# Performance work log

Measured on AMD Instinct MI355X. Metric: run time of the kernel, lower is better.

The kernel has to match this reference:

```python
import jax, jax.numpy as jnp
import numpy as np

# Emphasis(alpha=0.85): y[n] = x[n] - alpha*x[n-1], implemented (as in the original
# module) via a generic STFT-domain time-varying LFilter with n_fft=512, hop=256,
# normalization (torch.istft-style). Since n_fft == win_length, the per-frame
# convolution is circular within each frame, matching the original's framing.
N_FFT = 512
HOP = 256
WIN = 512
ALPHA = 0.85


def setup_inputs() -> dict:
    key = jax.random.key(0)
    x = jax.random.normal(key, (8, 1, 2097152), dtype=jnp.float32)
    coeffs = jnp.array([1.0, -ALPHA], dtype=jnp.float32)  # registered buffer [1, -alpha]
    return {"x": x, "coeffs": coeffs}


def _lfilter_fir(x, coeffs):
    # x: (B, C, T); coeffs: (2,) FIR numerator, constant across frames
    B, C, T = x.shape
    n_frames = -(-T // HOP)  # ceil_division(T, hop)
    pad_left = WIN // 2      # centered framing
    needed = (n_frames - 1) * HOP + WIN
    pad_right = max(needed - (pad_left + T), 0) + HOP
    xp = jnp.pad(x, ((0, 0), (0, 0), (pad_left, pad_right)))
    Lp = xp.shape[-1]

    n = jnp.arange(WIN, dtype=jnp.float32)
    window = 0.5 - 0.5 * jnp.cos(2.0 * jnp.pi * n / WIN)  # periodic Hann (torch.hann_window)

    idx = jnp.arange(n_frames)[:, None] * HOP + jnp.arange(WIN)[None, :]
    frames = xp[..., idx] * window

    X = jnp.fft.rfft(frames, n=N_FFT, axis=-1)         # (B, C, F, N_FFT//2+1)
    Bf = jnp.fft.rfft(coeffs, n=N_FFT)                 # (N_FFT//2+1,) same for every frame
    Y = X * Bf                                         # frequency-domain FIR
    yf = jnp.fft.irfft(Y, n=N_FFT, axis=-1) * window   # synthesis window

    # overlap-add + COLA (window-square) normalization
    y = jnp.zeros((B, C, Lp), dtype=x.dtype).at[..., idx].add(yf)
    wsum = jnp.zeros((Lp,), dtype=x.dtype).at[idx].add(window * window)
    y = y / jnp.maximum(wsum, 1e-8)
    return y[..., pad_left:pad_left + T]


def reference(x, coeffs):
    return _lfilter_fir(x, coeffs)
```

## Files before the change

### kernel.cpp

```cpp
#include <hip/hip_runtime.h>


constexpr int T_ROW = 1 << 21;
constexpr float ALPHA_C = 0.85f;

__global__ __launch_bounds__(256) void emphasis_kernel(
    const float* __restrict__ x, float* __restrict__ y, int nvec_total)
{
    __shared__ float sB[256];
    __shared__ float sAt[256];
    __shared__ float sBt[256];

    {
        const int m = threadIdx.x;
        const float fm = (float)m;
        const float s    = sinpif(fm * (1.0f / 512.0f));
        const float c    = cospif(fm * (1.0f / 512.0f));
        const float wm    = s * s;
        const float wm256 = c * c;
        const float s1    = sinpif((fm - 1.0f) * (1.0f / 512.0f));
        const float wm1   = s1 * s1;
        const float s255  = sinpif((fm + 255.0f) * (1.0f / 512.0f));
        const float wm255 = s255 * s255;

        const float A  = wm * wm + wm256 * wm256;
        const float Bc = wm * wm1 + wm256 * wm255;
        sB[m] = (-ALPHA_C * Bc) / fmaxf(A, 1e-8f);

        const float wn2 = wm256 * wm256;
        const float d   = fmaxf(wn2, 1e-8f);
        sAt[m] = wn2 / d;
        sBt[m] = (-ALPHA_C * wm256 * wm255) / d;
    }
    __syncthreads();

    const int stride = gridDim.x * blockDim.x;
    for (int v = blockIdx.x * blockDim.x + threadIdx.x; v < nvec_total; v += stride) {
        const long long i = (long long)v * 4;
        const int irow = (int)(i & (long long)(T_ROW - 1));
        const float4 xv = *reinterpret_cast<const float4*>(x + i);
        const float xm1 = (irow == 0) ? 0.0f : x[i - 1];
        const int m = irow & 255;
        float4 out;
        if (irow >= T_ROW - 256) {
            out.x = sAt[m + 0] * xv.x + sBt[m + 0] * xm1;
            out.y = sAt[m + 1] * xv.y + sBt[m + 1] * xv.x;
            out.z = sAt[m + 2] * xv.z + sBt[m + 2] * xv.y;
            out.w = sAt[m + 3] * xv.w + sBt[m + 3] * xv.z;
        } else {
            out.x = xv.x + sB[m + 0] * xm1;
            out.y = xv.y + sB[m + 1] * xv.x;
            out.z = xv.z + sB[m + 2] * xv.y;
            out.w = xv.w + sB[m + 3] * xv.z;
        }
        *reinterpret_cast<float4*>(y + i) = out;
    }
}

extern "C" void kernel_launch(void* const* d_in, const int* in_sizes, int n_in,
                              void* d_out, int out_size, void* d_ws, size_t ws_size,
                              hipStream_t stream) {
    const float* x = (const float*)d_in[0];
    float* y = (float*)d_out;
    const int nvec = out_size / 4;
    const int block = 256;
    int grid = (nvec + block - 1) / block;
    if (grid > 2048) grid = 2048;
    emphasis_kernel<<<grid, block, 0, stream>>>(x, y, nvec);
}
```

Before: 114.6 us.

## Compute coefficients in registers per thread and loop over batch rows

The kernel drops the shared-memory coefficient tables and the grid-stride loop. Each thread now owns one 4-sample column position within a row, computes its own coefficients in registers once, and reuses them across all 8 batch rows. The previous sample now comes from a wavefront shuffle instead of a second global load, except at lane 0. The cost is redundant transcendental work per thread and a fixed grid of 2048 blocks, each doing 8 iterations. The shape is hardcoded to 8 rows.

```diff
diff --git a/kernel.cpp b/kernel.cpp
--- a/kernel.cpp
+++ b/kernel.cpp
@@ -2,58 +2,58 @@
 
 
 constexpr int T_ROW = 1 << 21;
+constexpr int N_ROWS = 8;
 constexpr float ALPHA_C = 0.85f;
 
+typedef float f32x4 __attribute__((ext_vector_type(4)));
+
 __global__ __launch_bounds__(256) void emphasis_kernel(
-    const float* __restrict__ x, float* __restrict__ y, int nvec_total)
+    const float* __restrict__ x, float* __restrict__ y)
 {
-    __shared__ float sB[256];
-    __shared__ float sAt[256];
-    __shared__ float sBt[256];
+    const int tid = blockIdx.x * 256 + threadIdx.x;
+    const long long off = (long long)tid * 4;
+    const int m = (int)(off & 255);
 
-    {
-        const int m = threadIdx.x;
-        const float fm = (float)m;
-        const float s    = sinpif(fm * (1.0f / 512.0f));
-        const float c    = cospif(fm * (1.0f / 512.0f));
+    float cA[4], cB[4];
+    const bool tail = (off >= (long long)(T_ROW - 256));
+    #pragma unroll
+    for (int j = 0; j < 4; ++j) {
+        const float fm = (float)(m + j);
+        const float s     = sinpif(fm * (1.0f / 512.0f));
+        const float c     = cospif(fm * (1.0f / 512.0f));
         const float wm    = s * s;
         const float wm256 = c * c;
         const float s1    = sinpif((fm - 1.0f) * (1.0f / 512.0f));
         const float wm1   = s1 * s1;
         const float s255  = sinpif((fm + 255.0f) * (1.0f / 512.0f));
         const float wm255 = s255 * s255;
+        if (tail) {
+            const float wn2 = wm256 * wm256;
+            const float d   = fmaxf(wn2, 1e-8f);
+            cA[j] = wn2 / d;
+            cB[j] = (-ALPHA_C * wm256 * wm255) / d;
+        } else {
+            const float A = fmaxf(wm * wm + wm256 * wm256, 1e-8f);
+            cA[j] = 1.0f;
+            cB[j] = (-ALPHA_C * (wm * wm1 + wm256 * wm255)) / A;
+        }
+    }
 
-        const float A  = wm * wm + wm256 * wm256;
-        const float Bc = wm * wm1 + wm256 * wm255;
-        sB[m] = (-ALPHA_C * Bc) / fmaxf(A, 1e-8f);
-
-        const float wn2 = wm256 * wm256;
-        const float d   = fmaxf(wn2, 1e-8f);
-        sAt[m] = wn2 / d;
-        sBt[m] = (-ALPHA_C * wm256 * wm255) / d;
-    }
-    __syncthreads();
-
-    const int stride = gridDim.x * blockDim.x;
-    for (int v = blockIdx.x * blockDim.x + threadIdx.x; v < nvec_total; v += stride) {
-        const long long i = (long long)v * 4;
-        const int irow = (int)(i & (long long)(T_ROW - 1));
-        const float4 xv = *reinterpret_cast<const float4*>(x + i);
-        const float xm1 = (irow == 0) ? 0.0f : x[i - 1];
-        const int m = irow & 255;
-        float4 out;
-        if (irow >= T_ROW - 256) {
-            out.x = sAt[m + 0] * xv.x + sBt[m + 0] * xm1;
-            out.y = sAt[m + 1] * xv.y + sBt[m + 1] * xv.x;
-            out.z = sAt[m + 2] * xv.z + sBt[m + 2] * xv.y;
-            out.w = sAt[m + 3] * xv.w + sBt[m + 3] * xv.z;
-        } else {
-            out.x = xv.x + sB[m + 0] * xm1;
-            out.y = xv.y + sB[m + 1] * xv.x;
-            out.z = xv.z + sB[m + 2] * xv.y;
-            out.w = xv.w + sB[m + 3] * xv.z;
-        }
-        *reinterpret_cast<float4*>(y + i) = out;
+    const int lane = threadIdx.x & 63;
+    const float* xr = x + off;
+    float* yr = y + off;
+    #pragma unroll
+    for (int b = 0; b < N_ROWS; ++b) {
+        const long long ro = (long long)b * T_ROW;
+        const f32x4 xv = *reinterpret_cast<const f32x4*>(xr + ro);
+        float xm1 = __shfl_up(xv.w, 1);
+        if (lane == 0) xm1 = (off == 0) ? 0.0f : xr[ro - 1];
+        f32x4 o;
+        o.x = cA[0] * xv.x + cB[0] * xm1;
+        o.y = cA[1] * xv.y + cB[1] * xv.x;
+        o.z = cA[2] * xv.z + cB[2] * xv.y;
+        o.w = cA[3] * xv.w + cB[3] * xv.z;
+        *reinterpret_cast<f32x4*>(yr + ro) = o;
     }
 }
 
@@ -62,9 +62,8 @@
                               hipStream_t stream) {
     const float* x = (const float*)d_in[0];
     float* y = (float*)d_out;
-    const int nvec = out_size / 4;
+    const int nthreads = T_ROW / 4;
     const int block = 256;
-    int grid = (nvec + block - 1) / block;
-    if (grid > 2048) grid = 2048;
-    emphasis_kernel<<<grid, block, 0, stream>>>(x, y, nvec);
+    const int grid = nthreads / block;
+    emphasis_kernel<<<grid, block, 0, stream>>>(x, y);
 }
```

Result: no change. 115.5 us (+0.7%).
